# Optimization experiments

Measured on AMD Instinct MI355X. Metric: run time of the kernel, lower is better.

## Reference

```python
import jax, jax.numpy as jnp
import numpy as np

B, S, H, MAX_STEP = 128, 1024, 256, 10
NEG_INF = -1e8


def setup_inputs() -> dict:
    key = jax.random.key(0)
    ks = jax.random.split(key, 16)
    sc = 0.05
    return {
        "s0": jax.random.normal(ks[0], (B, H), jnp.float32),
        "h0": jax.random.normal(ks[1], (B, H), jnp.float32),
        "doc_encoding": jax.random.normal(ks[2], (B, S, H), jnp.float32),
        "W_ih": jax.random.normal(ks[3], (3 * H, H), jnp.float32) * sc,
        "W_hh": jax.random.normal(ks[4], (3 * H, H), jnp.float32) * sc,
        "b_ih": jax.random.normal(ks[5], (3 * H,), jnp.float32) * sc,
        "b_hh": jax.random.normal(ks[6], (3 * H,), jnp.float32) * sc,
        "Wq": jax.random.normal(ks[7], (H, H), jnp.float32) * sc,
        "bq": jax.random.normal(ks[8], (H,), jnp.float32) * sc,
        "Wd": jax.random.normal(ks[9], (H, H), jnp.float32) * sc,
        "bd": jax.random.normal(ks[10], (H,), jnp.float32) * sc,
        "Ws": jax.random.normal(ks[11], (1, H), jnp.float32) * sc,
        "bs": jax.random.normal(ks[12], (1,), jnp.float32) * sc,
        "tgt": jax.random.randint(ks[13], (B, MAX_STEP), 0, S, jnp.int64 if jax.config.jax_enable_x64 else jnp.int32),
        "sent_length": jax.random.randint(ks[14], (B,), 1, S + 1, jnp.int64 if jax.config.jax_enable_x64 else jnp.int32),
    }


def reference(s0, h0, doc_encoding, W_ih, W_hh, b_ih, b_hh, Wq, bq, Wd, bd, Ws, bs, tgt, sent_length):
    batch, sent_len, hid = doc_encoding.shape
    # padding mask: 1 where position >= doc length
    mask = (jnp.arange(sent_len)[None, :] >= sent_length[:, None]).astype(doc_encoding.dtype)  # [B,S]
    # precomputed attention keys: linear_d(context)
    precompute = jnp.einsum('bsh,kh->bsk', doc_encoding, Wd) + bd  # [B,S,H]
    # teacher-forced indices (original maps -1 -> 0)
    tgt_idx = jnp.where(tgt == -1, 0, tgt)  # [B,T]
    batch_ar = jnp.arange(batch)

    def gru_cell(x, h):
        gi = x @ W_ih.T + b_ih  # [B,3H]
        gh = h @ W_hh.T + b_hh
        i_r, i_z, i_n = jnp.split(gi, 3, axis=-1)
        h_r, h_z, h_n = jnp.split(gh, 3, axis=-1)
        r = jax.nn.sigmoid(i_r + h_r)
        z = jax.nn.sigmoid(i_z + h_z)
        n = jnp.tanh(i_n + r * h_n)
        return (1.0 - z) * n + z * h

    def step(carry, idx_t):
        cur_input, h = carry
        h = gru_cell(cur_input, h)
        target = h @ Wq.T + bq  # [B,H]
        energy = jnp.squeeze(jnp.tanh(precompute + target[:, None, :]) @ Ws.T, -1) + bs[0]  # [B,S]
        energy = energy * (1.0 - mask) + mask * NEG_INF
        cur_next = doc_encoding[batch_ar, idx_t]  # hard-attention gather [B,H]
        return (cur_next, h), energy

    _, all_score = jax.lax.scan(step, (s0, h0), tgt_idx.T)  # [T,B,S]
    return all_score, mask
```

## Files before the change

### kernel.cpp

```cpp
#include <hip/hip_runtime.h>

typedef unsigned short ushort_t;
typedef unsigned int uint_t;
typedef __attribute__((ext_vector_type(8))) short short8;
typedef __attribute__((ext_vector_type(4))) float f32x4;

#define B_   128
#define S_   1024
#define H_   256
#define T_   10
#define NEG_INF_ -1e8f

static __device__ __forceinline__ ushort_t f2bf(float x) {
    unsigned int u = __float_as_uint(x);
    unsigned int r = u + 0x7FFFu + ((u >> 16) & 1u);
    return (ushort_t)(r >> 16);
}
static __device__ __forceinline__ float bflo(uint_t w) {
    return __uint_as_float(w << 16);
}
static __device__ __forceinline__ float bfhi(uint_t w) {
    return __uint_as_float(w & 0xFFFF0000u);
}
static __device__ __forceinline__ float sigf(float x) {
    return 1.0f / (1.0f + __expf(-x));
}
static __device__ __forceinline__ float tanh_acc(float x) {
    return 2.0f / (1.0f + __expf(-2.0f * x)) - 1.0f;
}
static __device__ __forceinline__ float tanh_fast(float x) {
    float u = x * x;
    float p = fmaf(0.019063f, u, -0.18852f);
    p = fmaf(p, u, 0.93106f);
    float r = x * p;
    return __builtin_amdgcn_fmed3f(r, -1.0f, 1.0f);
}
static __device__ __forceinline__ short8 pack_bf8(float4 a, float4 b) {
    short8 r;
    r[0] = (short)f2bf(a.x); r[1] = (short)f2bf(a.y);
    r[2] = (short)f2bf(a.z); r[3] = (short)f2bf(a.w);
    r[4] = (short)f2bf(b.x); r[5] = (short)f2bf(b.y);
    r[6] = (short)f2bf(b.z); r[7] = (short)f2bf(b.w);
    return r;
}

__global__ void prep_transpose(const float* __restrict__ W_ih,
                               const float* __restrict__ W_hh,
                               const float* __restrict__ Wq,
                               uint_t* __restrict__ planes) {
    __shared__ float lds[64][65];
    const int p = blockIdx.x >> 4, tile = blockIdx.x & 15;
    const int j0 = (tile >> 2) * 64, c0 = (tile & 3) * 64;
    const float* src;
    if (p < 3)      src = W_ih + (size_t)p * 65536;
    else if (p < 6) src = W_hh + (size_t)(p - 3) * 65536;
    else            src = Wq;
    uint_t* dst = planes + (size_t)p * 32768;
    const int tid = threadIdx.x;
#pragma unroll
    for (int p4 = 0; p4 < 4; ++p4) {
        int i = p4 * 256 + tid;
        int jj = i >> 4, cc4 = (i & 15) * 4;
        float4 v = *((const float4*)&src[(size_t)(j0 + jj) * 256 + c0 + cc4]);
        lds[jj][cc4]     = v.x;
        lds[jj][cc4 + 1] = v.y;
        lds[jj][cc4 + 2] = v.z;
        lds[jj][cc4 + 3] = v.w;
    }
    __syncthreads();
#pragma unroll
    for (int p8 = 0; p8 < 8; ++p8) {
        int i = p8 * 256 + tid;
        int c2 = i >> 6, j = i & 63;
        float lo = lds[j][c2 * 2], hi = lds[j][c2 * 2 + 1];
        uint_t val = (uint_t)f2bf(lo) | ((uint_t)f2bf(hi) << 16);
        dst[(size_t)(c0 / 2 + c2) * 256 + j0 + j] = val;
    }
}

__global__ void prep_small(const float* __restrict__ Wd, const int* __restrict__ slen,
                           ushort_t* __restrict__ Wd_bf, float* __restrict__ out_mask) {
    int i = blockIdx.x * 256 + threadIdx.x;
    if (i < 65536) { Wd_bf[i] = f2bf(Wd[i]); return; }
    i -= 65536;
    int b = i >> 10, s = i & 1023;
    out_mask[i] = (s >= slen[b]) ? 1.0f : 0.0f;
}

__global__ __launch_bounds__(512) void gru_all(
        const float* __restrict__ s0, const float* __restrict__ h0,
        const float* __restrict__ doc, const int* __restrict__ tgt,
        const uint_t* __restrict__ planes, const float* __restrict__ b_ih,
        const float* __restrict__ b_hh, const float* __restrict__ bq,
        float* __restrict__ targets) {
    __shared__ float xs[T_][256];
    __shared__ float hs[256];
    __shared__ float pr[256], pz[256], pn[256], pq[256];
    const int b = blockIdx.x;
    const int tid = threadIdx.x;
    const int j = tid & 255, half = tid >> 8;

    const uint_t* ihr = planes;
    const uint_t* ihz = planes + 32768;
    const uint_t* ihn = planes + 2 * 32768;
    const uint_t* hhr = planes + 3 * 32768;
    const uint_t* hhz = planes + 4 * 32768;
    const uint_t* hhn = planes + 5 * 32768;
    const uint_t* qT  = planes + 6 * 32768;

    for (int i = tid; i < 640; i += 512) {
        int t = i >> 6, c4 = i & 63;
        const float* src;
        if (t == 0) src = s0 + (size_t)b * H_;
        else {
            int idx = tgt[b * T_ + t - 1];
            if (idx < 0) idx = 0;
            src = doc + ((size_t)b * S_ + idx) * H_;
        }
        ((float4*)&xs[t][0])[c4] = ((const float4*)src)[c4];
    }
    if (half == 0) hs[j] = h0[(size_t)b * H_ + j];
    const float bhr = b_hh[j], bhz = b_hh[j + 256], bhn = b_hh[j + 512];
    const float bqj = bq[j];
    const float bihr = b_ih[j], bihz = b_ih[j + 256], bihn = b_ih[j + 512];
    __syncthreads();

    float g_r[5], g_z[5], g_n[5];
#pragma unroll
    for (int u = 0; u < 5; ++u) { g_r[u] = bihr; g_z[u] = bihz; g_n[u] = bihn; }
    const int tbase = half * 5;
#pragma unroll 1
    for (int bb = 0; bb < 16; ++bb) {
        uint_t wr8[8], wz8[8], wn8[8];
#pragma unroll
        for (int v = 0; v < 8; ++v) {
            int c2 = bb * 8 + v;
            wr8[v] = ihr[c2 * 256 + j];
            wz8[v] = ihz[c2 * 256 + j];
            wn8[v] = ihn[c2 * 256 + j];
        }
#pragma unroll
        for (int v = 0; v < 8; ++v) {
            int c2 = bb * 8 + v;
            float wr0 = bflo(wr8[v]), wr1 = bfhi(wr8[v]);
            float wz0 = bflo(wz8[v]), wz1 = bfhi(wz8[v]);
            float wn0 = bflo(wn8[v]), wn1 = bfhi(wn8[v]);
#pragma unroll
            for (int u = 0; u < 5; ++u) {
                float2 x2 = *((const float2*)&xs[tbase + u][c2 * 2]);
                g_r[u] = fmaf(wr0, x2.x, g_r[u]); g_r[u] = fmaf(wr1, x2.y, g_r[u]);
                g_z[u] = fmaf(wz0, x2.x, g_z[u]); g_z[u] = fmaf(wz1, x2.y, g_z[u]);
                g_n[u] = fmaf(wn0, x2.x, g_n[u]); g_n[u] = fmaf(wn1, x2.y, g_n[u]);
            }
        }
    }

    const int c2base = half * 64;
    const uint_t* hhr_h = hhr + (size_t)c2base * 256 + j;
    const uint_t* hhz_h = hhz + (size_t)c2base * 256 + j;
    const uint_t* hhn_h = hhn + (size_t)c2base * 256 + j;
    const uint_t* qT_h  = qT  + (size_t)c2base * 256 + j;

#pragma unroll
    for (int t = 0; t < T_; ++t) {
        const bool holder = (half == (t >= 5 ? 1 : 0));
        const int u = (t < 5) ? t : t - 5;
        float ar = 0.f, az = 0.f, an = 0.f;
#pragma unroll 1
        for (int bb = 0; bb < 8; ++bb) {
            uint_t wr8[8], wz8[8], wn8[8];
#pragma unroll
            for (int v = 0; v < 8; ++v) {
                int c2i = bb * 8 + v;
                wr8[v] = hhr_h[c2i * 256];
                wz8[v] = hhz_h[c2i * 256];
                wn8[v] = hhn_h[c2i * 256];
            }
#pragma unroll
            for (int v = 0; v < 8; ++v) {
                int c2i = bb * 8 + v;
                float2 h2 = *((const float2*)&hs[(c2base + c2i) * 2]);
                ar = fmaf(bflo(wr8[v]), h2.x, ar); ar = fmaf(bfhi(wr8[v]), h2.y, ar);
                az = fmaf(bflo(wz8[v]), h2.x, az); az = fmaf(bfhi(wz8[v]), h2.y, az);
                an = fmaf(bflo(wn8[v]), h2.x, an); an = fmaf(bfhi(wn8[v]), h2.y, an);
            }
        }
        if (!holder) { pr[j] = ar; pz[j] = az; pn[j] = an; }
        __syncthreads();
        if (holder) {
            float art = ar + pr[j] + bhr;
            float azt = az + pz[j] + bhz;
            float ant = an + pn[j] + bhn;
            float r = sigf(g_r[u] + art);
            float z = sigf(g_z[u] + azt);
            float n = tanh_acc(fmaf(r, ant, g_n[u]));
            float hold = hs[j];
            hs[j] = fmaf(z, hold - n, n);
        }
        __syncthreads();
        float q = 0.f;
#pragma unroll 1
        for (int bb = 0; bb < 4; ++bb) {
            uint_t wq16[16];
#pragma unroll
            for (int v = 0; v < 16; ++v)
                wq16[v] = qT_h[(bb * 16 + v) * 256];
#pragma unroll
            for (int v = 0; v < 16; ++v) {
                int c2i = bb * 16 + v;
                float2 h2 = *((const float2*)&hs[(c2base + c2i) * 2]);
                q = fmaf(bflo(wq16[v]), h2.x, q); q = fmaf(bfhi(wq16[v]), h2.y, q);
            }
        }
        if (!holder) pq[j] = q;
        __syncthreads();
        if (holder) targets[((size_t)t * B_ + b) * H_ + j] = q + pq[j] + bqj;
    }
}

__global__ __launch_bounds__(256, 3) void energy_kernel(
        const float* __restrict__ doc, const ushort_t* __restrict__ Wd_bf,
        const float* __restrict__ targets, const float* __restrict__ bd,
        const float* __restrict__ Ws, const float* __restrict__ bs,
        const int* __restrict__ slenp, float* __restrict__ out) {
    __shared__ float tg[T_][256];
    __shared__ float ws_l[256], bd_l[256];
    const int bid = blockIdx.x;
    const int b = bid >> 3, st = bid & 7;
    const int tid = threadIdx.x;

    for (int i = tid; i < 640; i += 256) {
        int t = i >> 6, k4 = i & 63;
        ((float4*)&tg[t][0])[k4] = *((const float4*)&targets[((size_t)t * B_ + b) * H_ + k4 * 4]);
    }
    if (tid < 64) ((float4*)ws_l)[tid] = ((const float4*)Ws)[tid];
    else if (tid < 128) ((float4*)bd_l)[tid - 64] = ((const float4*)bd)[tid - 64];

    const int lane = tid & 63, w = tid >> 6;
    const int r16 = lane & 15, g = lane >> 4;

    const int s0_loc = st * 128 + w * 16 + r16;
    const float* drow0 = doc + ((size_t)b * S_ + s0_loc) * H_ + g * 8;
    const float* drow1 = drow0 + (size_t)64 * H_;
    short8 bdoc0[8], bdoc1[8];
#pragma unroll
    for (int ks = 0; ks < 8; ++ks) {
        float4 v0 = *((const float4*)(drow0 + ks * 32));
        float4 v1 = *((const float4*)(drow0 + ks * 32 + 4));
        bdoc0[ks] = pack_bf8(v0, v1);
        float4 u0 = *((const float4*)(drow1 + ks * 32));
        float4 u1 = *((const float4*)(drow1 + ks * 32 + 4));
        bdoc1[ks] = pack_bf8(u0, u1);
    }
    __syncthreads();

    float e0[T_], e1[T_];
#pragma unroll
    for (int t = 0; t < T_; ++t) { e0[t] = 0.f; e1[t] = 0.f; }

    const ushort_t* wbase = Wd_bf + (size_t)r16 * H_ + g * 8;
    const int kq = g * 4;

#pragma unroll 2
    for (int nt = 0; nt < 16; ++nt) {
        const int k0 = nt * 16 + kq;
        const ushort_t* wrow = wbase + (size_t)(nt * 16) * H_;
        short8 awd[8];
#pragma unroll
        for (int ks = 0; ks < 8; ++ks) awd[ks] = *((const short8*)(wrow + ks * 32));
        f32x4 bd4 = *((const f32x4*)&bd_l[k0]);
        f32x4 a00 = bd4;
        f32x4 a01 = {0.f, 0.f, 0.f, 0.f};
        f32x4 a10 = bd4;
        f32x4 a11 = {0.f, 0.f, 0.f, 0.f};
#pragma unroll
        for (int ks = 0; ks < 4; ++ks) {
            a00 = __builtin_amdgcn_mfma_f32_16x16x32_bf16(awd[ks],     bdoc0[ks],     a00, 0, 0, 0);
            a01 = __builtin_amdgcn_mfma_f32_16x16x32_bf16(awd[ks + 4], bdoc0[ks + 4], a01, 0, 0, 0);
            a10 = __builtin_amdgcn_mfma_f32_16x16x32_bf16(awd[ks],     bdoc1[ks],     a10, 0, 0, 0);
            a11 = __builtin_amdgcn_mfma_f32_16x16x32_bf16(awd[ks + 4], bdoc1[ks + 4], a11, 0, 0, 0);
        }
        f32x4 pA = a00 + a01;
        f32x4 pB = a10 + a11;
        f32x4 ws4 = *((const f32x4*)&ws_l[k0]);
#pragma unroll
        for (int t = 0; t < T_; ++t) {
            f32x4 tg4 = *((const f32x4*)&tg[t][k0]);
#pragma unroll
            for (int rr = 0; rr < 4; ++rr) {
                e0[t] = fmaf(tanh_fast(pA[rr] + tg4[rr]), ws4[rr], e0[t]);
                e1[t] = fmaf(tanh_fast(pB[rr] + tg4[rr]), ws4[rr], e1[t]);
            }
        }
    }

#pragma unroll
    for (int t = 0; t < T_; ++t) {
        e0[t] += __shfl_xor(e0[t], 16);
        e0[t] += __shfl_xor(e0[t], 32);
        e1[t] += __shfl_xor(e1[t], 16);
        e1[t] += __shfl_xor(e1[t], 32);
    }

    const int slen = slenp[b];
    const float bs0 = bs[0];
    const bool pad0 = (s0_loc >= slen);
    const bool pad1 = (s0_loc + 64 >= slen);
    float* obase = out + (size_t)b * S_ + s0_loc;
#pragma unroll
    for (int tt = g; tt < T_; tt += 4) {
        obase[(size_t)tt * B_ * S_]      = pad0 ? NEG_INF_ : (e0[tt] + bs0);
        obase[(size_t)tt * B_ * S_ + 64] = pad1 ? NEG_INF_ : (e1[tt] + bs0);
    }
}

extern "C" void kernel_launch(void* const* d_in, const int* in_sizes, int n_in,
                              void* d_out, int out_size, void* d_ws, size_t ws_size,
                              hipStream_t stream) {
    (void)in_sizes; (void)n_in; (void)out_size; (void)ws_size;
    const float* s0   = (const float*)d_in[0];
    const float* h0   = (const float*)d_in[1];
    const float* doc  = (const float*)d_in[2];
    const float* W_ih = (const float*)d_in[3];
    const float* W_hh = (const float*)d_in[4];
    const float* b_ih = (const float*)d_in[5];
    const float* b_hh = (const float*)d_in[6];
    const float* Wq   = (const float*)d_in[7];
    const float* bq   = (const float*)d_in[8];
    const float* Wd   = (const float*)d_in[9];
    const float* bd   = (const float*)d_in[10];
    const float* Ws   = (const float*)d_in[11];
    const float* bs   = (const float*)d_in[12];
    const int*   tgt  = (const int*)d_in[13];
    const int*   slen = (const int*)d_in[14];

    float* out_score = (float*)d_out;
    float* out_mask  = out_score + T_ * B_ * S_;

    char* ws = (char*)d_ws;
    uint_t*   planes  = (uint_t*)(ws + 0);
    ushort_t* Wd_bf   = (ushort_t*)(ws + 917504);
    float*    targets = (float*)(ws + 1048576);

    prep_transpose<<<112, 256, 0, stream>>>(W_ih, W_hh, Wq, planes);
    prep_small<<<768, 256, 0, stream>>>(Wd, slen, Wd_bf, out_mask);
    gru_all<<<128, 512, 0, stream>>>(s0, h0, doc, tgt, planes, b_ih, b_hh, bq, targets);
    energy_kernel<<<1024, 256, 0, stream>>>(doc, Wd_bf, targets, bd, Ws, bs, slen, out_score);
}
```

Measured before the change: 179.0 us.

## Split energy kernel hidden dimension across wave pairs with LDS reduction

The energy kernel now uses 2048 blocks of 64 sequence rows each. Within a block, two waves cover the same rows but each takes half of the 256 output columns of Wd, and their partial energies are added through shared memory before writing. The bias bd is folded into the target vectors in shared memory, so it no longer seeds the MFMA accumulators. This doubles the block count and halves per-wave work, aiming for more parallelism and latency hiding. The cost is that each doc row is now loaded and converted by two waves, plus an extra barrier and LDS reduction.

```diff
diff --git a/kernel.cpp b/kernel.cpp
--- a/kernel.cpp
+++ b/kernel.cpp
@@ -224,24 +224,29 @@
         const float* __restrict__ Ws, const float* __restrict__ bs,
         const int* __restrict__ slenp, float* __restrict__ out) {
     __shared__ float tg[T_][256];
-    __shared__ float ws_l[256], bd_l[256];
+    __shared__ float ws_l[256];
+    __shared__ float eparts[2][16][T_][2];
     const int bid = blockIdx.x;
-    const int b = bid >> 3, st = bid & 7;
+    const int b = bid >> 4, st = bid & 15;
     const int tid = threadIdx.x;
 
     for (int i = tid; i < 640; i += 256) {
         int t = i >> 6, k4 = i & 63;
-        ((float4*)&tg[t][0])[k4] = *((const float4*)&targets[((size_t)t * B_ + b) * H_ + k4 * 4]);
+        float4 tv = *((const float4*)&targets[((size_t)t * B_ + b) * H_ + k4 * 4]);
+        float4 bv = *((const float4*)&bd[k4 * 4]);
+        tv.x += bv.x; tv.y += bv.y; tv.z += bv.z; tv.w += bv.w;
+        ((float4*)&tg[t][0])[k4] = tv;
     }
     if (tid < 64) ((float4*)ws_l)[tid] = ((const float4*)Ws)[tid];
-    else if (tid < 128) ((float4*)bd_l)[tid - 64] = ((const float4*)bd)[tid - 64];
 
     const int lane = tid & 63, w = tid >> 6;
     const int r16 = lane & 15, g = lane >> 4;
-
-    const int s0_loc = st * 128 + w * 16 + r16;
+    const int rw = w & 1;
+    const int nh = w >> 1;
+
+    const int s0_loc = st * 64 + rw * 16 + r16;
     const float* drow0 = doc + ((size_t)b * S_ + s0_loc) * H_ + g * 8;
-    const float* drow1 = drow0 + (size_t)64 * H_;
+    const float* drow1 = drow0 + (size_t)32 * H_;
     short8 bdoc0[8], bdoc1[8];
 #pragma unroll
     for (int ks = 0; ks < 8; ++ks) {
@@ -261,17 +266,17 @@
     const ushort_t* wbase = Wd_bf + (size_t)r16 * H_ + g * 8;
     const int kq = g * 4;
 
-#pragma unroll 2
-    for (int nt = 0; nt < 16; ++nt) {
+#pragma unroll 1
+    for (int i = 0; i < 8; ++i) {
+        const int nt = nh * 8 + i;
         const int k0 = nt * 16 + kq;
         const ushort_t* wrow = wbase + (size_t)(nt * 16) * H_;
         short8 awd[8];
 #pragma unroll
         for (int ks = 0; ks < 8; ++ks) awd[ks] = *((const short8*)(wrow + ks * 32));
-        f32x4 bd4 = *((const f32x4*)&bd_l[k0]);
-        f32x4 a00 = bd4;
+        f32x4 a00 = {0.f, 0.f, 0.f, 0.f};
         f32x4 a01 = {0.f, 0.f, 0.f, 0.f};
-        f32x4 a10 = bd4;
+        f32x4 a10 = {0.f, 0.f, 0.f, 0.f};
         f32x4 a11 = {0.f, 0.f, 0.f, 0.f};
 #pragma unroll
         for (int ks = 0; ks < 4; ++ks) {
@@ -302,15 +307,27 @@
         e1[t] += __shfl_xor(e1[t], 32);
     }
 
-    const int slen = slenp[b];
-    const float bs0 = bs[0];
-    const bool pad0 = (s0_loc >= slen);
-    const bool pad1 = (s0_loc + 64 >= slen);
-    float* obase = out + (size_t)b * S_ + s0_loc;
-#pragma unroll
-    for (int tt = g; tt < T_; tt += 4) {
-        obase[(size_t)tt * B_ * S_]      = pad0 ? NEG_INF_ : (e0[tt] + bs0);
-        obase[(size_t)tt * B_ * S_ + 64] = pad1 ? NEG_INF_ : (e1[tt] + bs0);
+    if (nh == 1 && g == 0) {
+#pragma unroll
+        for (int t = 0; t < T_; ++t) {
+            eparts[rw][r16][t][0] = e0[t];
+            eparts[rw][r16][t][1] = e1[t];
+        }
+    }
+    __syncthreads();
+    if (nh == 0) {
+        const int slen = slenp[b];
+        const float bs0 = bs[0];
+        const bool pad0 = (s0_loc >= slen);
+        const bool pad1 = (s0_loc + 32 >= slen);
+        float* obase = out + (size_t)b * S_ + s0_loc;
+#pragma unroll
+        for (int tt = g; tt < T_; tt += 4) {
+            float v0 = e0[tt] + eparts[rw][r16][tt][0] + bs0;
+            float v1 = e1[tt] + eparts[rw][r16][tt][1] + bs0;
+            obase[(size_t)tt * B_ * S_]      = pad0 ? NEG_INF_ : v0;
+            obase[(size_t)tt * B_ * S_ + 32] = pad1 ? NEG_INF_ : v1;
+        }
     }
 }
 
@@ -345,5 +362,5 @@
     prep_transpose<<<112, 256, 0, stream>>>(W_ih, W_hh, Wq, planes);
     prep_small<<<768, 256, 0, stream>>>(Wd, slen, Wd_bf, out_mask);
     gru_all<<<128, 512, 0, stream>>>(s0, h0, doc, tgt, planes, b_ih, b_hh, bq, targets);
-    energy_kernel<<<1024, 256, 0, stream>>>(doc, Wd_bf, targets, bd, Ws, bs, slen, out_score);
-}
+    energy_kernel<<<2048, 256, 0, stream>>>(doc, Wd_bf, targets, bd, Ws, bs, slen, out_score);
+}
```

Measured after the change: 185.5 us. +3.6%, slower.
